# Performance work log

Hardware: AMD Instinct MI355X
Metric: run time of the kernel (lower is better)

Reference implementation:

```python
import jax, jax.numpy as jnp
import numpy as np

N, E, B = 100000, 640000, 256
F_IN, HID, HEADS = 128, 128, 4
C = HID // HEADS  # 32 channels per head
NEG_SLOPE = 0.2


def _p(key, shape, scale=0.1):
    return (jax.random.normal(key, shape) * scale).astype(jnp.float32)


def setup_inputs() -> dict:
    key = jax.random.key(0)
    ks = jax.random.split(key, 24)
    inp = {
        "x": jax.random.normal(ks[0], (N, F_IN), jnp.float32),
        "edge_index": jax.random.randint(ks[1], (2, E), 0, N),
        "batch": jnp.sort(jax.random.randint(ks[2], (N,), 0, B)),
        "w_in": _p(ks[3], (F_IN, HID)),
        "b_in": jnp.zeros((HID,), jnp.float32),
    }
    for i in range(3):
        inp[f"w{i}"] = _p(ks[4 + 4 * i], (HID, HEADS * C))
        inp[f"asrc{i}"] = _p(ks[5 + 4 * i], (HEADS, C))
        inp[f"adst{i}"] = _p(ks[6 + 4 * i], (HEADS, C))
        inp[f"b{i}"] = jnp.zeros((HID if i < 2 else C,), jnp.float32)
    inp["w_fp"] = _p(ks[20], (C, HID)); inp["b_fp"] = jnp.zeros((HID,), jnp.float32)
    inp["w_m1"] = _p(ks[21], (HID, HID // 2)); inp["b_m1"] = jnp.zeros((HID // 2,), jnp.float32)
    inp["w_m2"] = _p(ks[22], (HID // 2, 1)); inp["b_m2"] = jnp.zeros((1,), jnp.float32)
    return inp


def _gat(x, src, dst, W, a_src, a_dst, bias, concat):
    """PyG-style GATConv (edge_dim=None, eval mode, self-loops pre-appended)."""
    n = x.shape[0]
    H, Ch = a_src.shape
    h = (x @ W).reshape(n, H, Ch)                     # [N,H,C]
    al_s = (h * a_src).sum(-1)                        # [N,H]
    al_d = (h * a_dst).sum(-1)                        # [N,H]
    logit = jax.nn.leaky_relu(al_s[src] + al_d[dst], NEG_SLOPE)  # [Etot,H]
    # segment softmax over incoming edges of each dst node
    m = jax.ops.segment_max(logit, dst, num_segments=n)
    e = jnp.exp(logit - m[dst])
    s = jax.ops.segment_sum(e, dst, num_segments=n)
    alpha = e / (s[dst] + 1e-16)                      # [Etot,H]
    out = jax.ops.segment_sum(h[src] * alpha[:, :, None], dst, num_segments=n)  # [N,H,C]
    out = out.reshape(n, H * Ch) if concat else out.mean(axis=1)
    return out + bias


def reference(x, edge_index, batch, w_in, b_in,
              w0, asrc0, adst0, b0, w1, asrc1, adst1, b1, w2, asrc2, adst2, b2,
              w_fp, b_fp, w_m1, b_m1, w_m2, b_m2):
    n = x.shape[0]
    loops = jnp.arange(n, dtype=edge_index.dtype)
    src = jnp.concatenate([edge_index[0], loops])     # add self loops (PyG default)
    dst = jnp.concatenate([edge_index[1], loops])
    h = x @ w_in + b_in
    h = jax.nn.elu(_gat(h, src, dst, w0, asrc0, adst0, b0, True))
    h = jax.nn.elu(_gat(h, src, dst, w1, asrc1, adst1, b1, True))
    h = jax.nn.elu(_gat(h, src, dst, w2, asrc2, adst2, b2, False))  # [N,C]
    cnt = jax.ops.segment_sum(jnp.ones((n,), h.dtype), batch, num_segments=B)
    pooled = jax.ops.segment_sum(h, batch, num_segments=B) / jnp.maximum(cnt, 1.0)[:, None]
    out = pooled @ w_fp + b_fp                        # final_proj (out dim 32 != 128)
    hm = jax.nn.relu(out @ w_m1 + b_m1)
    return hm @ w_m2 + b_m2                           # [B,1]
```

## Files before the change

kernel.cpp:

```cpp
#include <hip/hip_runtime.h>

#define NEG 0.2f

typedef short s16x8 __attribute__((ext_vector_type(8)));
typedef float f32x4 __attribute__((ext_vector_type(4)));

__device__ __forceinline__ float lrelu(float x) { return x >= 0.f ? x : NEG * x; }
__device__ __forceinline__ float elu1(float x) { return x > 0.f ? x : __expf(x) - 1.f; }

__device__ __forceinline__ unsigned bf16rn(float f) {
    unsigned u = __float_as_uint(f);
    u += 0x7fffu + ((u >> 16) & 1u);
    return u >> 16;
}
__device__ __forceinline__ float bf16tof(ushort h) {
    return __uint_as_float(((unsigned)h) << 16);
}
__device__ __forceinline__ float bf16lo(unsigned u) { return __uint_as_float(u << 16); }
__device__ __forceinline__ float bf16hi(unsigned u) { return __uint_as_float(u & 0xffff0000u); }

__global__ void hist_kernel(const int* __restrict__ dst, int e, int n, int* __restrict__ deg) {
    int p = blockIdx.x & 7;
    int s = blockIdx.x >> 3;
    int nslices = gridDim.x >> 3;
    int rng = (n + 7) >> 3;
    int lo = p * rng, hi = min(n, lo + rng);
    int chunk = (e + nslices - 1) / nslices;
    int i0 = s * chunk, i1 = min(e, i0 + chunk);
    for (int i = i0 + threadIdx.x; i < i1; i += blockDim.x) {
        int d = dst[i];
        if (d >= lo && d < hi) atomicAdd(&deg[d], 1);
    }
}

__device__ __forceinline__ int waveIncScanI(int v, int lane) {
#pragma unroll
    for (int off = 1; off < 64; off <<= 1) {
        int u = __shfl_up(v, off);
        if (lane >= off) v += u;
    }
    return v;
}

__global__ void scan1_kernel(const int* __restrict__ deg, int nk,
                             int* __restrict__ rowp, int* __restrict__ bsums) {
    int t = threadIdx.x;
    int base = blockIdx.x * 2048 + t * 8;
    int vals[8];
    int sum = 0;
#pragma unroll
    for (int i = 0; i < 8; ++i) {
        int idx = base + i;
        int v = (idx < nk) ? deg[idx] : 0;
        vals[i] = sum;
        sum += v;
    }
    int lane = t & 63, w = t >> 6;
    int inc = waveIncScanI(sum, lane);
    __shared__ int wsums[4];
    if (lane == 63) wsums[w] = inc;
    __syncthreads();
    int wpre = 0;
#pragma unroll
    for (int i = 0; i < 3; ++i) wpre += (i < w) ? wsums[i] : 0;
    int exc = wpre + inc - sum;
#pragma unroll
    for (int i = 0; i < 8; ++i) {
        int idx = base + i;
        if (idx < nk) rowp[idx] = exc + vals[i];
    }
    if (t == 255) bsums[blockIdx.x] = wpre + inc;
}

__global__ void scan3_kernel(int* __restrict__ rowp, const int* __restrict__ bsums,
                             int nk, int total, int* __restrict__ cursor) {
    int g = blockIdx.x;
    __shared__ int spre;
    if (threadIdx.x < 64) {
        int lane = threadIdx.x;
        int v = 0;
        for (int base = lane; base < g; base += 64) v += bsums[base];
#pragma unroll
        for (int off = 32; off > 0; off >>= 1) v += __shfl_xor(v, off);
        if (lane == 0) spre = v;
    }
    __syncthreads();
    int pre = spre;
    int base = g * 2048 + threadIdx.x * 8;
#pragma unroll
    for (int i = 0; i < 8; ++i) {
        int idx = base + i;
        if (idx < nk) {
            int v = rowp[idx] + pre;
            rowp[idx] = v;
            cursor[idx] = v;
        } else if (idx == nk) {
            rowp[nk] = total;
        }
    }
}

__global__ void fill_kernel(const int* __restrict__ src, const int* __restrict__ dst, int e,
                            int n, int* __restrict__ cursor, int* __restrict__ col) {
    int p = blockIdx.x & 7;
    int s = blockIdx.x >> 3;
    int nslices = gridDim.x >> 3;
    int rng = (n + 7) >> 3;
    int lo = p * rng, hi = min(n, lo + rng);
    int chunk = (e + nslices - 1) / nslices;
    int i0 = s * chunk, i1 = min(e, i0 + chunk);
    for (int i = i0 + threadIdx.x; i < i1; i += blockDim.x) {
        int d = dst[i];
        if (d >= lo && d < hi) {
            int pos = atomicAdd(&cursor[d], 1);
            col[pos] = src[i];
        }
    }
}

__global__ void wpack_kernel(const float* __restrict__ w_in, const float* __restrict__ w0,
                             const float* __restrict__ w1, const float* __restrict__ w2,
                             const float* __restrict__ b_in,
                             ushort* __restrict__ whi, ushort* __restrict__ wlo,
                             float* __restrict__ beff, int n, int* __restrict__ degz) {
    int idx = blockIdx.x * 256 + threadIdx.x;
    int stride = gridDim.x * 256;
    for (int i = idx; i < n; i += stride) degz[i] = 0;
    if (idx >= 3 * 16384) return;
    int layer = idx >> 14, e = idx & 16383;
    int k = e >> 7, c = e & 127;
    float wv;
    if (layer == 0) {
        float s = 0.f;
        for (int m = 0; m < 128; ++m) s += w_in[k * 128 + m] * w0[m * 128 + c];
        wv = s;
    } else {
        const float* W = (layer == 1) ? w1 : w2;
        wv = W[e];
    }
    ushort hi = (ushort)bf16rn(wv);
    ushort lo = (ushort)bf16rn(wv - bf16tof(hi));
    int kt = k >> 5, kk = k & 31, j = kk & 7;
    int ln = ((kk >> 3) << 4) | (c & 15);
    int ntg = c >> 4;
    int pos = (layer << 14) + (((kt << 3) + ntg) * 64 + ln) * 8 + j;
    whi[pos] = hi;
    wlo[pos] = lo;
    if (idx < 128) {
        float s = 0.f;
        for (int m = 0; m < 128; ++m) s += b_in[m] * w0[m * 128 + idx];
        beff[idx] = s;
    }
}

template <bool BIAS, bool AL, bool ABF16>
__global__ __launch_bounds__(512, 2) void gemm_mfma_kernel(
    const void* __restrict__ Av, const ushort* __restrict__ whi, const ushort* __restrict__ wlo,
    const float* __restrict__ bias, ushort* __restrict__ outb, int n, int ntiles,
    const float* __restrict__ asrc, const float* __restrict__ adst,
    float* __restrict__ als, float* __restrict__ ald) {
    __shared__ s16x8 ahi[2][2][4][64];
    __shared__ s16x8 alo[2][2][4][64];
    int t = threadIdx.x;
    int wid = t >> 6, lane = t & 63;
    int ntp = wid & 3;
    int mhalf = wid >> 2;

    const s16x8* wph = (const s16x8*)whi;
    const s16x8* wpl = (const s16x8*)wlo;
    s16x8 wh[4][2], wl[4][2];
#pragma unroll
    for (int kt = 0; kt < 4; ++kt)
#pragma unroll
        for (int j = 0; j < 2; ++j) {
            int ntg = ntp * 2 + j;
            wh[kt][j] = wph[((kt << 3) + ntg) * 64 + lane];
            wl[kt][j] = wpl[((kt << 3) + ntg) * 64 + lane];
        }

    int c0 = ntp * 32 + (lane & 15);
    int c1 = c0 + 16;
    float bv0 = 0.f, bv1 = 0.f;
    if (BIAS) { bv0 = bias[c0]; bv1 = bias[c1]; }
    float as0 = 0.f, as1 = 0.f, ad0 = 0.f, ad1 = 0.f;
    if (AL) {
        as0 = asrc[ntp * 32 + (lane & 15)];
        as1 = asrc[ntp * 32 + 16 + (lane & 15)];
        ad0 = adst[ntp * 32 + (lane & 15)];
        ad1 = adst[ntp * 32 + 16 + (lane & 15)];
    }

    int srow = t >> 4, skoct = t & 15;
    int smh = srow >> 4, skt = skoct >> 2;
    int sln = ((skoct & 3) << 4) | (srow & 15);

    auto stage = [&](int tile, int bi) {
        int gr = tile * 32 + srow;
        if (ABF16) {
            const ushort* Ab = (const ushort*)Av;
            s16x8 hi = {0, 0, 0, 0, 0, 0, 0, 0};
            if (gr < n) hi = *(const s16x8*)(Ab + (size_t)gr * 128 + skoct * 8);
            ahi[bi][smh][skt][sln] = hi;
        } else {
            const float* Af = (const float*)Av;
            float4 v0 = make_float4(0.f, 0.f, 0.f, 0.f), v1 = v0;
            if (gr < n) {
                const float4* rp = (const float4*)(Af + (size_t)gr * 128 + skoct * 8);
                v0 = rp[0];
                v1 = rp[1];
            }
            float f[8] = {v0.x, v0.y, v0.z, v0.w, v1.x, v1.y, v1.z, v1.w};
            s16x8 hi, lo;
#pragma unroll
            for (int j = 0; j < 8; ++j) {
                ushort h = (ushort)bf16rn(f[j]);
                hi[j] = (short)h;
                lo[j] = (short)bf16rn(f[j] - bf16tof(h));
            }
            ahi[bi][smh][skt][sln] = hi;
            alo[bi][smh][skt][sln] = lo;
        }
    };

    int tile = blockIdx.x;
    if (tile < ntiles) stage(tile, 0);
    int cur = 0;
    __syncthreads();

    for (; tile < ntiles; tile += gridDim.x) {
        int nxt = tile + gridDim.x;
        if (nxt < ntiles) stage(nxt, cur ^ 1);

        f32x4 acc0 = {0.f, 0.f, 0.f, 0.f};
        f32x4 acc1 = {0.f, 0.f, 0.f, 0.f};
#pragma unroll
        for (int kt = 0; kt < 4; ++kt) {
            s16x8 ah = ahi[cur][mhalf][kt][lane];
            if (ABF16) {
                acc0 = __builtin_amdgcn_mfma_f32_16x16x32_bf16(ah, wh[kt][0], acc0, 0, 0, 0);
                acc0 = __builtin_amdgcn_mfma_f32_16x16x32_bf16(ah, wl[kt][0], acc0, 0, 0, 0);
                acc1 = __builtin_amdgcn_mfma_f32_16x16x32_bf16(ah, wh[kt][1], acc1, 0, 0, 0);
                acc1 = __builtin_amdgcn_mfma_f32_16x16x32_bf16(ah, wl[kt][1], acc1, 0, 0, 0);
            } else {
                s16x8 al = alo[cur][mhalf][kt][lane];
                acc0 = __builtin_amdgcn_mfma_f32_16x16x32_bf16(ah, wh[kt][0], acc0, 0, 0, 0);
                acc0 = __builtin_amdgcn_mfma_f32_16x16x32_bf16(ah, wl[kt][0], acc0, 0, 0, 0);
                acc0 = __builtin_amdgcn_mfma_f32_16x16x32_bf16(al, wh[kt][0], acc0, 0, 0, 0);
                acc1 = __builtin_amdgcn_mfma_f32_16x16x32_bf16(ah, wh[kt][1], acc1, 0, 0, 0);
                acc1 = __builtin_amdgcn_mfma_f32_16x16x32_bf16(ah, wl[kt][1], acc1, 0, 0, 0);
                acc1 = __builtin_amdgcn_mfma_f32_16x16x32_bf16(al, wh[kt][1], acc1, 0, 0, 0);
            }
        }

        int rbase = tile * 32 + mhalf * 16 + (lane >> 4) * 4;
#pragma unroll
        for (int i = 0; i < 4; ++i) {
            int r = rbase + i;
            float o0 = acc0[i] + bv0;
            float o1 = acc1[i] + bv1;
            if (r < n) {
                outb[(size_t)r * 128 + c0] = (ushort)bf16rn(o0);
                outb[(size_t)r * 128 + c1] = (ushort)bf16rn(o1);
            }
            if (AL) {
                float ps = o0 * as0 + o1 * as1;
                float pd = o0 * ad0 + o1 * ad1;
                ps += __shfl_xor(ps, 1); ps += __shfl_xor(ps, 2);
                ps += __shfl_xor(ps, 4); ps += __shfl_xor(ps, 8);
                pd += __shfl_xor(pd, 1); pd += __shfl_xor(pd, 2);
                pd += __shfl_xor(pd, 4); pd += __shfl_xor(pd, 8);
                if ((lane & 15) == 0 && r < n) {
                    als[r * 4 + ntp] = ps;
                    ald[r * 4 + ntp] = pd;
                }
            }
        }
        __syncthreads();
        cur ^= 1;
    }
}

template <bool CONCAT>
__global__ void agg_kernel(const ushort* __restrict__ hp, const float* __restrict__ als,
                           const float* __restrict__ ald_, const int* __restrict__ rowp,
                           const int* __restrict__ col, const float* __restrict__ bias,
                           ushort* __restrict__ outb, float* __restrict__ outf, int n) {
    int lane = threadIdx.x & 63;
    int hl = lane & 31;
    int wid = (blockIdx.x * blockDim.x + threadIdx.x) >> 6;
    int d = wid * 2 + (lane >> 5);
    bool valid = d < n;
    int dc = valid ? d : (n - 1);

    int h = hl >> 3;
    int c4 = hl * 4;
    int hh = hl & 3;
    int jl = hl >> 2;
    int bshf = lane & 32;

    int start = rowp[dc];
    int end = valid ? rowp[dc + 1] : start;

    float aldv_hh = ald_[dc * 4 + hh];
    float eself = __expf(lrelu(als[dc * 4 + h] + ald_[dc * 4 + h]));

    uint2 sv = *(const uint2*)(hp + (size_t)dc * 128 + c4);
    float a0 = eself * bf16lo(sv.x), a1 = eself * bf16hi(sv.x);
    float a2 = eself * bf16lo(sv.y), a3 = eself * bf16hi(sv.y);
    float esum = eself;

    int iters = (end - start + 7) >> 3;
    int oiters = __shfl_xor(iters, 32);
    int maxit = iters > oiters ? iters : oiters;
    unsigned nclamp = (unsigned)(n - 1);

    for (int it = 0; it < maxit; ++it) {
        int p0 = start + it * 8;
        bool act = p0 < end;
        int pc = act ? p0 : start;
        int4 ca = *(const int4*)(col + pc);
        int4 cb = *(const int4*)(col + pc + 4);
        int v0 = (jl & 4) ? cb.x : ca.x;
        int v1 = (jl & 4) ? cb.y : ca.y;
        int v2 = (jl & 4) ? cb.z : ca.z;
        int v3 = (jl & 4) ? cb.w : ca.w;
        int w0_ = (jl & 2) ? v2 : v0;
        int w1_ = (jl & 2) ? v3 : v1;
        unsigned se = (unsigned)((jl & 1) ? w1_ : w0_);
        se = se > nclamp ? nclamp : se;
        float ee = __expf(lrelu(als[(size_t)se * 4 + hh] + aldv_hh));
        ee = (act && (p0 + jl < end)) ? ee : 0.f;

#define EDGE(JJ, SRC)                                                              \
        {                                                                          \
            float ej = __shfl(ee, bshf | (JJ << 2) | h);                           \
            unsigned sju = (unsigned)(SRC);                                        \
            sju = sju > nclamp ? nclamp : sju;                                     \
            uint2 uv = *(const uint2*)(hp + (size_t)sju * 128 + c4);               \
            a0 += ej * bf16lo(uv.x); a1 += ej * bf16hi(uv.x);                      \
            a2 += ej * bf16lo(uv.y); a3 += ej * bf16hi(uv.y);                      \
            esum += ej;                                                            \
        }
        EDGE(0, ca.x) EDGE(1, ca.y) EDGE(2, ca.z) EDGE(3, ca.w)
        EDGE(4, cb.x) EDGE(5, cb.y) EDGE(6, cb.z) EDGE(7, cb.w)
#undef EDGE
    }

    float inv = 1.f / (esum + 1e-16f);
    a0 *= inv; a1 *= inv; a2 *= inv; a3 *= inv;
    if (CONCAT) {
        if (valid) {
            float o0 = elu1(a0 + bias[c4]);
            float o1 = elu1(a1 + bias[c4 + 1]);
            float o2 = elu1(a2 + bias[c4 + 2]);
            float o3 = elu1(a3 + bias[c4 + 3]);
            uint2 pk;
            pk.x = bf16rn(o0) | (bf16rn(o1) << 16);
            pk.y = bf16rn(o2) | (bf16rn(o3) << 16);
            *(uint2*)(outb + (size_t)d * 128 + c4) = pk;
        }
    } else {
        a0 += __shfl_xor(a0, 8); a0 += __shfl_xor(a0, 16);
        a1 += __shfl_xor(a1, 8); a1 += __shfl_xor(a1, 16);
        a2 += __shfl_xor(a2, 8); a2 += __shfl_xor(a2, 16);
        a3 += __shfl_xor(a3, 8); a3 += __shfl_xor(a3, 16);
        if (valid && hl < 8) {
            int cin = hl * 4;
            float4 o;
            o.x = elu1(a0 * 0.25f + bias[cin]);
            o.y = elu1(a1 * 0.25f + bias[cin + 1]);
            o.z = elu1(a2 * 0.25f + bias[cin + 2]);
            o.w = elu1(a3 * 0.25f + bias[cin + 3]);
            *(float4*)(outf + (size_t)d * 32 + cin) = o;
        }
    }
}

__global__ void poolmlp_kernel(const float* __restrict__ h2, const int* __restrict__ batch,
                               int n, const float* __restrict__ w_fp,
                               const float* __restrict__ b_fp, const float* __restrict__ w_m1,
                               const float* __restrict__ b_m1, const float* __restrict__ w_m2,
                               const float* __restrict__ b_m2, float* __restrict__ out) {
    int b = blockIdx.x, t = threadIdx.x;
    __shared__ int sb[2];
    if (t == 0) {
        int lo = 0, hi = n;
        while (lo < hi) { int mid = (lo + hi) >> 1; if (batch[mid] < b) lo = mid + 1; else hi = mid; }
        sb[0] = lo;
        int lo2 = lo, hi2 = n;
        while (lo2 < hi2) { int mid = (lo2 + hi2) >> 1; if (batch[mid] < b + 1) lo2 = mid + 1; else hi2 = mid; }
        sb[1] = lo2;
    }
    __syncthreads();
    int lo = sb[0], hi = sb[1];
    int c = t & 31, g = t >> 5;
    float acc = 0.f;
    for (int i = lo + g; i < hi; i += 8) acc += h2[(size_t)i * 32 + c];
    __shared__ float red[8][32];
    __shared__ float sp[32], so[128];
    red[g][c] = acc;
    __syncthreads();
    if (t < 32) {
        float s = 0.f;
#pragma unroll
        for (int g2 = 0; g2 < 8; ++g2) s += red[g2][t];
        float cnt = (float)(hi - lo);
        sp[t] = s / fmaxf(cnt, 1.f);
    }
    __syncthreads();
    if (t < 128) {
        float o = b_fp[t];
#pragma unroll 8
        for (int k = 0; k < 32; ++k) o += sp[k] * w_fp[k * 128 + t];
        so[t] = o;
    }
    __syncthreads();
    if (t < 64) {
        float hm = b_m1[t];
        for (int cc = 0; cc < 128; ++cc) hm += so[cc] * w_m1[cc * 64 + t];
        float v = fmaxf(hm, 0.f) * w_m2[t];
#pragma unroll
        for (int offd = 32; offd > 0; offd >>= 1) v += __shfl_down(v, offd);
        if (t == 0) out[b] = v + b_m2[0];
    }
}

extern "C" void kernel_launch(void* const* d_in, const int* in_sizes, int n_in,
                              void* d_out, int out_size, void* d_ws, size_t ws_size,
                              hipStream_t stream) {
    const float* x = (const float*)d_in[0];
    const int* ei = (const int*)d_in[1];
    const int* batch = (const int*)d_in[2];
    const float* w_in = (const float*)d_in[3];
    const float* b_in = (const float*)d_in[4];
    const float* w[3] = {(const float*)d_in[5], (const float*)d_in[9], (const float*)d_in[13]};
    const float* asrc[3] = {(const float*)d_in[6], (const float*)d_in[10], (const float*)d_in[14]};
    const float* adst[3] = {(const float*)d_in[7], (const float*)d_in[11], (const float*)d_in[15]};
    const float* bb[3] = {(const float*)d_in[8], (const float*)d_in[12], (const float*)d_in[16]};
    const float* w_fp = (const float*)d_in[17];
    const float* b_fp = (const float*)d_in[18];
    const float* w_m1 = (const float*)d_in[19];
    const float* b_m1 = (const float*)d_in[20];
    const float* w_m2 = (const float*)d_in[21];
    const float* b_m2 = (const float*)d_in[22];

    int n = in_sizes[0] / 128;
    int e = in_sizes[1] / 2;
    int B = out_size;

    char* wsb = (char*)d_ws;
    size_t off = 0;
    auto alloc = [&](size_t bytes) -> void* {
        void* p = wsb + off;
        off += (bytes + 255) & ~(size_t)255;
        return p;
    };
    ushort* hAu = (ushort*)alloc((size_t)n * 128 * 2);
    ushort* hBu = (ushort*)alloc((size_t)n * 128 * 2);
    float* h3 = (float*)alloc((size_t)n * 32 * 4);
    float* als = (float*)alloc((size_t)n * 4 * 4);
    float* ald = (float*)alloc((size_t)n * 4 * 4);
    int* deg = (int*)alloc((size_t)n * 4);
    int* rowp = (int*)alloc((size_t)(n + 1) * 4);
    int* col = (int*)alloc((size_t)(e + 8) * 4);
    int* bsums = (int*)alloc(4096);
    ushort* whi = (ushort*)alloc((size_t)3 * 16384 * 2);
    ushort* wlo = (ushort*)alloc((size_t)3 * 16384 * 2);
    float* beff = (float*)alloc(128 * 4);

    const int* srcp = ei;
    const int* dstp = ei + e;

    wpack_kernel<<<192, 256, 0, stream>>>(w_in, w[0], w[1], w[2], b_in, whi, wlo, beff,
                                          n, deg);

    hist_kernel<<<1024, 256, 0, stream>>>(dstp, e, n, deg);
    int nb = (n + 2047) / 2048;
    scan1_kernel<<<nb, 256, 0, stream>>>(deg, n, rowp, bsums);
    scan3_kernel<<<nb, 256, 0, stream>>>(rowp, bsums, n, e, deg);
    fill_kernel<<<1024, 256, 0, stream>>>(srcp, dstp, e, n, deg, col);

    int ntiles = (n + 31) / 32;
    int gblk = ntiles < 512 ? ntiles : 512;
    int gridAgg = (n + 7) / 8;

    gemm_mfma_kernel<true, true, false><<<gblk, 512, 0, stream>>>(
        x, whi, wlo, beff, hBu, n, ntiles, asrc[0], adst[0], als, ald);
    agg_kernel<true><<<gridAgg, 256, 0, stream>>>(hBu, als, ald, rowp, col, bb[0],
                                                  hAu, nullptr, n);

    for (int L = 1; L < 3; ++L) {
        gemm_mfma_kernel<false, true, true><<<gblk, 512, 0, stream>>>(
            hAu, whi + (size_t)L * 16384, wlo + (size_t)L * 16384, nullptr, hBu, n,
            ntiles, asrc[L], adst[L], als, ald);
        if (L < 2)
            agg_kernel<true><<<gridAgg, 256, 0, stream>>>(hBu, als, ald, rowp, col, bb[L],
                                                          hAu, nullptr, n);
        else
            agg_kernel<false><<<gridAgg, 256, 0, stream>>>(hBu, als, ald, rowp, col, bb[L],
                                                           nullptr, h3, n);
    }

    poolmlp_kernel<<<B, 256, 0, stream>>>(h3, batch, n, w_fp, b_fp, w_m1, b_m1, w_m2, b_m2,
                                          (float*)d_out);
}
```

Baseline: 282.7 us.

## Fuse CSR build and weight packing into one cooperative kernel with grid syncs

Merges the weight-pack, degree histogram, two scan passes and CSR fill kernels into a single cooperative launch, separated by grid-wide barriers. This removes four kernel launches and the gaps between them. In exchange it adds grid.sync costs and requires all 1024 blocks of 256 threads to be co-resident. On this GPU that should fit, but it limits how the scheduler can run the blocks.

```diff
diff --git a/kernel.cpp b/kernel.cpp
--- a/kernel.cpp
+++ b/kernel.cpp
@@ -1,4 +1,7 @@
 #include <hip/hip_runtime.h>
+#include <hip/hip_cooperative_groups.h>
+
+namespace cg = cooperative_groups;
 
 #define NEG 0.2f
 
@@ -19,20 +22,6 @@
 __device__ __forceinline__ float bf16lo(unsigned u) { return __uint_as_float(u << 16); }
 __device__ __forceinline__ float bf16hi(unsigned u) { return __uint_as_float(u & 0xffff0000u); }
 
-__global__ void hist_kernel(const int* __restrict__ dst, int e, int n, int* __restrict__ deg) {
-    int p = blockIdx.x & 7;
-    int s = blockIdx.x >> 3;
-    int nslices = gridDim.x >> 3;
-    int rng = (n + 7) >> 3;
-    int lo = p * rng, hi = min(n, lo + rng);
-    int chunk = (e + nslices - 1) / nslices;
-    int i0 = s * chunk, i1 = min(e, i0 + chunk);
-    for (int i = i0 + threadIdx.x; i < i1; i += blockDim.x) {
-        int d = dst[i];
-        if (d >= lo && d < hi) atomicAdd(&deg[d], 1);
-    }
-}
-
 __device__ __forceinline__ int waveIncScanI(int v, int lane) {
 #pragma unroll
     for (int off = 1; off < 64; off <<= 1) {
@@ -42,114 +31,138 @@
     return v;
 }
 
-__global__ void scan1_kernel(const int* __restrict__ deg, int nk,
-                             int* __restrict__ rowp, int* __restrict__ bsums) {
-    int t = threadIdx.x;
-    int base = blockIdx.x * 2048 + t * 8;
-    int vals[8];
-    int sum = 0;
-#pragma unroll
-    for (int i = 0; i < 8; ++i) {
-        int idx = base + i;
-        int v = (idx < nk) ? deg[idx] : 0;
-        vals[i] = sum;
-        sum += v;
-    }
-    int lane = t & 63, w = t >> 6;
-    int inc = waveIncScanI(sum, lane);
-    __shared__ int wsums[4];
-    if (lane == 63) wsums[w] = inc;
-    __syncthreads();
-    int wpre = 0;
-#pragma unroll
-    for (int i = 0; i < 3; ++i) wpre += (i < w) ? wsums[i] : 0;
-    int exc = wpre + inc - sum;
-#pragma unroll
-    for (int i = 0; i < 8; ++i) {
-        int idx = base + i;
-        if (idx < nk) rowp[idx] = exc + vals[i];
-    }
-    if (t == 255) bsums[blockIdx.x] = wpre + inc;
-}
-
-__global__ void scan3_kernel(int* __restrict__ rowp, const int* __restrict__ bsums,
-                             int nk, int total, int* __restrict__ cursor) {
-    int g = blockIdx.x;
-    __shared__ int spre;
-    if (threadIdx.x < 64) {
-        int lane = threadIdx.x;
-        int v = 0;
-        for (int base = lane; base < g; base += 64) v += bsums[base];
-#pragma unroll
-        for (int off = 32; off > 0; off >>= 1) v += __shfl_xor(v, off);
-        if (lane == 0) spre = v;
-    }
-    __syncthreads();
-    int pre = spre;
-    int base = g * 2048 + threadIdx.x * 8;
-#pragma unroll
-    for (int i = 0; i < 8; ++i) {
-        int idx = base + i;
-        if (idx < nk) {
-            int v = rowp[idx] + pre;
-            rowp[idx] = v;
-            cursor[idx] = v;
-        } else if (idx == nk) {
-            rowp[nk] = total;
-        }
-    }
-}
-
-__global__ void fill_kernel(const int* __restrict__ src, const int* __restrict__ dst, int e,
-                            int n, int* __restrict__ cursor, int* __restrict__ col) {
-    int p = blockIdx.x & 7;
-    int s = blockIdx.x >> 3;
-    int nslices = gridDim.x >> 3;
-    int rng = (n + 7) >> 3;
-    int lo = p * rng, hi = min(n, lo + rng);
-    int chunk = (e + nslices - 1) / nslices;
-    int i0 = s * chunk, i1 = min(e, i0 + chunk);
-    for (int i = i0 + threadIdx.x; i < i1; i += blockDim.x) {
-        int d = dst[i];
-        if (d >= lo && d < hi) {
-            int pos = atomicAdd(&cursor[d], 1);
-            col[pos] = src[i];
-        }
-    }
-}
-
-__global__ void wpack_kernel(const float* __restrict__ w_in, const float* __restrict__ w0,
-                             const float* __restrict__ w1, const float* __restrict__ w2,
-                             const float* __restrict__ b_in,
-                             ushort* __restrict__ whi, ushort* __restrict__ wlo,
-                             float* __restrict__ beff, int n, int* __restrict__ degz) {
-    int idx = blockIdx.x * 256 + threadIdx.x;
-    int stride = gridDim.x * 256;
-    for (int i = idx; i < n; i += stride) degz[i] = 0;
-    if (idx >= 3 * 16384) return;
-    int layer = idx >> 14, e = idx & 16383;
-    int k = e >> 7, c = e & 127;
-    float wv;
-    if (layer == 0) {
-        float s = 0.f;
-        for (int m = 0; m < 128; ++m) s += w_in[k * 128 + m] * w0[m * 128 + c];
-        wv = s;
-    } else {
-        const float* W = (layer == 1) ? w1 : w2;
-        wv = W[e];
-    }
-    ushort hi = (ushort)bf16rn(wv);
-    ushort lo = (ushort)bf16rn(wv - bf16tof(hi));
-    int kt = k >> 5, kk = k & 31, j = kk & 7;
-    int ln = ((kk >> 3) << 4) | (c & 15);
-    int ntg = c >> 4;
-    int pos = (layer << 14) + (((kt << 3) + ntg) * 64 + ln) * 8 + j;
-    whi[pos] = hi;
-    wlo[pos] = lo;
-    if (idx < 128) {
-        float s = 0.f;
-        for (int m = 0; m < 128; ++m) s += b_in[m] * w0[m * 128 + idx];
-        beff[idx] = s;
+__global__ void coopbuild_kernel(const int* __restrict__ src, const int* __restrict__ dst,
+                                 int e, int n,
+                                 const float* __restrict__ w_in, const float* __restrict__ w0,
+                                 const float* __restrict__ w1, const float* __restrict__ w2,
+                                 const float* __restrict__ b_in,
+                                 ushort* __restrict__ whi, ushort* __restrict__ wlo,
+                                 float* __restrict__ beff,
+                                 int* __restrict__ deg, int* __restrict__ rowp,
+                                 int* __restrict__ col, int* __restrict__ bsums) {
+    cg::grid_group grid = cg::this_grid();
+    int b = blockIdx.x, t = threadIdx.x;
+    int gid = b * 256 + t;
+    int gstride = gridDim.x * 256;
+    int nb = (n + 2047) / 2048;
+
+    for (int i = gid; i < n; i += gstride) deg[i] = 0;
+    if (gid < 3 * 16384) {
+        int layer = gid >> 14, ee = gid & 16383;
+        int k = ee >> 7, c = ee & 127;
+        float wv;
+        if (layer == 0) {
+            float s = 0.f;
+            for (int m = 0; m < 128; ++m) s += w_in[k * 128 + m] * w0[m * 128 + c];
+            wv = s;
+        } else {
+            const float* W = (layer == 1) ? w1 : w2;
+            wv = W[ee];
+        }
+        ushort hi = (ushort)bf16rn(wv);
+        ushort lo = (ushort)bf16rn(wv - bf16tof(hi));
+        int kt = k >> 5, kk = k & 31, j = kk & 7;
+        int ln = ((kk >> 3) << 4) | (c & 15);
+        int ntg = c >> 4;
+        int pos = (layer << 14) + (((kt << 3) + ntg) * 64 + ln) * 8 + j;
+        whi[pos] = hi;
+        wlo[pos] = lo;
+        if (gid < 128) {
+            float s = 0.f;
+            for (int m = 0; m < 128; ++m) s += b_in[m] * w0[m * 128 + gid];
+            beff[gid] = s;
+        }
+    }
+    __threadfence();
+    grid.sync();
+
+    {
+        int p = b & 7, s = b >> 3;
+        int nslices = gridDim.x >> 3;
+        int rng = (n + 7) >> 3;
+        int lo = p * rng, hi = min(n, lo + rng);
+        int chunk = (e + nslices - 1) / nslices;
+        int i0 = s * chunk, i1 = min(e, i0 + chunk);
+        for (int i = i0 + t; i < i1; i += 256) {
+            int d = dst[i];
+            if (d >= lo && d < hi) atomicAdd(&deg[d], 1);
+        }
+    }
+    __threadfence();
+    grid.sync();
+
+    if (b < nb) {
+        int base = b * 2048 + t * 8;
+        int vals[8];
+        int sum = 0;
+#pragma unroll
+        for (int i = 0; i < 8; ++i) {
+            int idx = base + i;
+            int v = (idx < n) ? deg[idx] : 0;
+            vals[i] = sum;
+            sum += v;
+        }
+        int lane = t & 63, w = t >> 6;
+        int inc = waveIncScanI(sum, lane);
+        __shared__ int wsums[4];
+        if (lane == 63) wsums[w] = inc;
+        __syncthreads();
+        int wpre = 0;
+#pragma unroll
+        for (int i = 0; i < 3; ++i) wpre += (i < w) ? wsums[i] : 0;
+        int exc = wpre + inc - sum;
+#pragma unroll
+        for (int i = 0; i < 8; ++i) {
+            int idx = base + i;
+            if (idx < n) rowp[idx] = exc + vals[i];
+        }
+        if (t == 255) bsums[b] = wpre + inc;
+    }
+    __threadfence();
+    grid.sync();
+
+    if (b < nb) {
+        __shared__ int spre;
+        if (t < 64) {
+            int lane = t;
+            int v = 0;
+            for (int base = lane; base < b; base += 64) v += bsums[base];
+#pragma unroll
+            for (int off = 32; off > 0; off >>= 1) v += __shfl_xor(v, off);
+            if (lane == 0) spre = v;
+        }
+        __syncthreads();
+        int pre = spre;
+        int base = b * 2048 + t * 8;
+#pragma unroll
+        for (int i = 0; i < 8; ++i) {
+            int idx = base + i;
+            if (idx < n) {
+                int v = rowp[idx] + pre;
+                rowp[idx] = v;
+                deg[idx] = v;
+            } else if (idx == n) {
+                rowp[n] = e;
+            }
+        }
+    }
+    __threadfence();
+    grid.sync();
+
+    {
+        int p = b & 7, s = b >> 3;
+        int nslices = gridDim.x >> 3;
+        int rng = (n + 7) >> 3;
+        int lo = p * rng, hi = min(n, lo + rng);
+        int chunk = (e + nslices - 1) / nslices;
+        int i0 = s * chunk, i1 = min(e, i0 + chunk);
+        for (int i = i0 + t; i < i1; i += 256) {
+            int d = dst[i];
+            if (d >= lo && d < hi) {
+                int pos = atomicAdd(&deg[d], 1);
+                col[pos] = src[i];
+            }
+        }
     }
 }
 
@@ -470,15 +483,18 @@
 
     const int* srcp = ei;
     const int* dstp = ei + e;
-
-    wpack_kernel<<<192, 256, 0, stream>>>(w_in, w[0], w[1], w[2], b_in, whi, wlo, beff,
-                                          n, deg);
-
-    hist_kernel<<<1024, 256, 0, stream>>>(dstp, e, n, deg);
-    int nb = (n + 2047) / 2048;
-    scan1_kernel<<<nb, 256, 0, stream>>>(deg, n, rowp, bsums);
-    scan3_kernel<<<nb, 256, 0, stream>>>(rowp, bsums, n, e, deg);
-    fill_kernel<<<1024, 256, 0, stream>>>(srcp, dstp, e, n, deg, col);
+    const float* w0p = w[0];
+    const float* w1p = w[1];
+    const float* w2p = w[2];
+
+    {
+        void* params[] = {(void*)&srcp, (void*)&dstp, (void*)&e, (void*)&n,
+                          (void*)&w_in, (void*)&w0p, (void*)&w1p, (void*)&w2p, (void*)&b_in,
+                          (void*)&whi, (void*)&wlo, (void*)&beff,
+                          (void*)&deg, (void*)&rowp, (void*)&col, (void*)&bsums};
+        hipLaunchCooperativeKernel((const void*)coopbuild_kernel, dim3(1024), dim3(256),
+                                   params, 0, stream);
+    }
 
     int ntiles = (n + 31) / 32;
     int gblk = ntiles < 512 ? ntiles : 512;
```

Result: slower. 931.5 us (+229.5%).
